# Kernel tuning notes

Measured on AMD Instinct MI355X. Metric: run time of the kernel, lower is better.

## Reference

```python
import jax, jax.numpy as jnp
import numpy as np

DIM = 256
WIN = 8          # window height == width
HEADS = 8
HEAD_DIM = DIM // HEADS
NW = 64          # number of windows per image
B_IMG = 16
N = WIN * WIN    # 64 tokens per window
B_ = B_IMG * NW  # 1024


def _relative_position_index():
    # matches torch.meshgrid default (ij) indexing
    coords = np.stack(np.meshgrid(np.arange(WIN), np.arange(WIN), indexing='ij'))  # [2,Wh,Ww]
    flat = coords.reshape(2, -1)                                # [2,N]
    rel = flat[:, :, None] - flat[:, None, :]                   # [2,N,N]
    rel = rel.transpose(1, 2, 0).copy()                         # [N,N,2]
    rel[:, :, 0] += WIN - 1
    rel[:, :, 1] += WIN - 1
    rel[:, :, 0] *= 2 * WIN - 1
    return rel.sum(-1).astype(np.int32)                         # [N,N]


def setup_inputs() -> dict:
    key = jax.random.key(0)
    ks = jax.random.split(key, 24)
    std = 0.02

    def lin(i):
        W = jax.random.normal(ks[i], (DIM, DIM), jnp.float32) * std
        b = jax.random.normal(ks[i + 1], (DIM,), jnp.float32) * std
        return W, b

    Wq, bq = lin(0)
    Wk, bk = lin(2)
    Wv, bv = lin(4)
    Wvs, bvs = lin(6)      # v_scale
    Wvh, bvh = lin(8)      # v_shift
    Wpx, bpx = lin(10)     # proj_x
    Wps, bps = lin(12)     # proj_scale
    Wph, bph = lin(14)     # proj_shift

    bias_table = jax.random.normal(ks[16], ((2 * WIN - 1) * (2 * WIN - 1), HEADS), jnp.float32) * std
    rel_idx = jnp.asarray(_relative_position_index())

    q_input = jax.random.normal(ks[17], (B_, N, DIM), jnp.float32)
    k_input = jax.random.normal(ks[18], (B_, N, DIM), jnp.float32)
    v_input = jax.random.normal(ks[19], (B_, N, DIM), jnp.float32)
    scale_in = jax.random.normal(ks[20], (B_, N, DIM), jnp.float32)
    shift_in = jax.random.normal(ks[21], (B_, N, DIM), jnp.float32)

    # shifted-window style mask: 0 where attendable, large negative otherwise
    u = jax.random.uniform(ks[22], (NW, N, N), jnp.float32)
    mask = jnp.where(u < 0.15, -100.0, 0.0).astype(jnp.float32)

    return {
        'q_input': q_input, 'k_input': k_input, 'v_input': v_input,
        'scale_in': scale_in, 'shift_in': shift_in, 'mask': mask,
        'Wq': Wq, 'bq': bq, 'Wk': Wk, 'bk': bk, 'Wv': Wv, 'bv': bv,
        'Wvs': Wvs, 'bvs': bvs, 'Wvh': Wvh, 'bvh': bvh,
        'Wpx': Wpx, 'bpx': bpx, 'Wps': Wps, 'bps': bps, 'Wph': Wph, 'bph': bph,
        'bias_table': bias_table, 'rel_idx': rel_idx,
    }


def reference(q_input, k_input, v_input, scale_in, shift_in, mask,
              Wq, bq, Wk, bk, Wv, bv, Wvs, bvs, Wvh, bvh,
              Wpx, bpx, Wps, bps, Wph, bph, bias_table, rel_idx):
    B, Ntok, C = q_input.shape
    scale = HEAD_DIM ** -0.5

    def to_heads(x, W, b):
        # nn.Linear: x @ W.T + b, then split heads -> [B, H, N, hd]
        return (x @ W.T + b).reshape(B, Ntok, HEADS, HEAD_DIM).transpose(0, 2, 1, 3)

    q = to_heads(q_input, Wq, bq) * scale
    k = to_heads(k_input, Wk, bk)
    v = to_heads(v_input, Wv, bv)
    v_scale = to_heads(scale_in, Wvs, bvs)
    v_shift = to_heads(shift_in, Wvh, bvh)

    attn = jnp.einsum('bhnd,bhmd->bhnm', q, k)                    # [B,H,N,N]
    rel_bias = bias_table[rel_idx]                                # [N,N,H] gather
    attn = attn + rel_bias.transpose(2, 0, 1)[None]               # add per-head bias

    nW = mask.shape[0]
    attn = attn.reshape(B // nW, nW, HEADS, Ntok, Ntok) + mask[None, :, None]
    attn = jax.nn.softmax(attn.reshape(B, HEADS, Ntok, Ntok), axis=-1)

    def out_proj(val, Wp, bp):
        o = jnp.einsum('bhnm,bhmd->bhnd', attn, val)
        o = o.transpose(0, 2, 1, 3).reshape(B, Ntok, C)
        return o @ Wp.T + bp

    x_out = out_proj(v, Wpx, bpx)
    scale_out = out_proj(v_scale, Wps, bps)
    shift_out = out_proj(v_shift, Wph, bph)
    return (x_out, scale_out, shift_out)
```

## Files before the change

### kernel.cpp

```cpp
#include <hip/hip_runtime.h>


typedef __attribute__((ext_vector_type(8))) __bf16 bf16x8;
typedef __attribute__((ext_vector_type(4))) float f32x4;
typedef __attribute__((ext_vector_type(4))) unsigned short u16x4;

__device__ __forceinline__ unsigned short f2bf(float f) {
  return __builtin_bit_cast(unsigned short, (__bf16)f);
}
__device__ __forceinline__ unsigned pk2(float lo, float hi) {
  return (unsigned)f2bf(lo) | ((unsigned)f2bf(hi) << 16);
}
__device__ __forceinline__ int swz256(int row, int col) {
  return row * 256 + (col ^ ((row & 31) << 3));
}
__device__ __forceinline__ f32x4 mfma16(bf16x8 a, bf16x8 b, f32x4 c) {
  return __builtin_amdgcn_mfma_f32_16x16x32_bf16(a, b, c, 0, 0, 0);
}

__global__ void pack_weights(const float* __restrict__ W0, const float* __restrict__ W1,
                             const float* __restrict__ W2, const float* __restrict__ W3,
                             const float* __restrict__ W4, const float* __restrict__ W5,
                             const float* __restrict__ W6, const float* __restrict__ W7,
                             unsigned short* __restrict__ pk) {
  int t = blockIdx.x * 256 + threadIdx.x;
  int mat = t >> 13;
  int w   = (t >> 11) & 3;
  int blk = (t >> 9) & 3;
  int kc  = (t >> 6) & 7;
  int l   = t & 63;
  const float* W = (mat == 0) ? W0 : (mat == 1) ? W1 : (mat == 2) ? W2 : (mat == 3) ? W3
                 : (mat == 4) ? W4 : (mat == 5) ? W5 : (mat == 6) ? W6 : W7;
  const float* src = W + (64 * w + 16 * blk + (l & 15)) * 256 + 32 * kc + 8 * (l >> 4);
  unsigned short* dst = pk + (size_t)t * 8;
#pragma unroll
  for (int i = 0; i < 8; ++i) dst[i] = f2bf(src[i]);
}

__global__ void make_bmt(const float* __restrict__ mask, const float* __restrict__ btab,
                         const int* __restrict__ ridx, float* __restrict__ bmt) {
  int t = blockIdx.x * 256 + threadIdx.x;
  int r  = t & 3;
  int l  = (t >> 2) & 63;
  int mf = (t >> 8) & 3;
  int nf = (t >> 10) & 3;
  int h  = (t >> 12) & 7;
  int wi = t >> 15;
  int q = 16 * nf + (l & 15);
  int k = 16 * mf + 4 * (l >> 4) + r;
  bmt[t] = mask[(wi * 64 + q) * 64 + k] + btab[ridx[q * 64 + k] * 8 + h];
}

__device__ __forceinline__ bf16x8 butterfly(f32x4 C0, f32x4 C1, int c4, int r16) {
  unsigned a0 = pk2(C0[0], C0[1]), a1 = pk2(C0[2], C0[3]);
  unsigned b0 = pk2(C1[0], C1[1]), b1 = pk2(C1[2], C1[3]);
  int src0 = (((2 * c4) & 3) << 4) + r16;
  int src1 = (((2 * c4 + 1) & 3) << 4) + r16;
  unsigned A0 = (unsigned)__shfl((int)a0, src0);
  unsigned A1 = (unsigned)__shfl((int)a1, src0);
  unsigned A2 = (unsigned)__shfl((int)a0, src1);
  unsigned A3 = (unsigned)__shfl((int)a1, src1);
  unsigned B0 = (unsigned)__shfl((int)b0, src0);
  unsigned B1 = (unsigned)__shfl((int)b1, src0);
  unsigned B2 = (unsigned)__shfl((int)b0, src1);
  unsigned B3 = (unsigned)__shfl((int)b1, src1);
  bool hi = c4 >= 2;
  union { unsigned u[4]; bf16x8 v; } r;
  r.u[0] = hi ? B0 : A0;
  r.u[1] = hi ? B1 : A1;
  r.u[2] = hi ? B2 : A2;
  r.u[3] = hi ? B3 : A3;
  return r.v;
}

__device__ __forceinline__ void load8(f32x4 r[8], const float* __restrict__ X,
                                      int b, int tid, int half) {
  const f32x4* src = reinterpret_cast<const f32x4*>(X + (size_t)b * 16384) + half * 2048;
#pragma unroll
  for (int it = 0; it < 8; ++it) r[it] = src[it * 256 + tid];
}
__device__ __forceinline__ void write8(unsigned short* T, const f32x4 r[8], int tid, int half) {
#pragma unroll
  for (int it = 0; it < 8; ++it) {
    int f = half * 2048 + it * 256 + tid;
    int row = f >> 6;
    int col = (f & 63) << 2;
    u16x4 p;
    p[0] = f2bf(r[it][0]); p[1] = f2bf(r[it][1]);
    p[2] = f2bf(r[it][2]); p[3] = f2bf(r[it][3]);
    *reinterpret_cast<u16x4*>(T + swz256(row, col)) = p;
  }
}
__device__ __forceinline__ void stage_tile(unsigned short* T, const float* __restrict__ X,
                                           int b, int tid) {
  f32x4 r[8];
  load8(r, X, b, tid, 0);
  write8(T, r, tid, 0);
  load8(r, X, b, tid, 1);
  write8(T, r, tid, 1);
}

__device__ __forceinline__ const unsigned short* pwBase(const unsigned short* pk,
                                                        int mat, int w2) {
  return pk + mat * 65536 + w2 * 16384;
}

__device__ __forceinline__ void projT2(const unsigned short* __restrict__ T,
                                       const unsigned short* __restrict__ pw,
                                       const float* __restrict__ bias, float scale,
                                       int lane, int w2, bf16x8 fA[4], bf16x8 fB[4]) {
  const int r16 = lane & 15, c4 = lane >> 4;
  f32x4 z = {0.f, 0.f, 0.f, 0.f};
  f32x4 acc[4][4];
#pragma unroll
  for (int j = 0; j < 4; ++j)
#pragma unroll
    for (int nf = 0; nf < 4; ++nf) acc[j][nf] = z;
#pragma unroll
  for (int kc = 0; kc < 8; ++kc) {
    bf16x8 aw[4], bx[4];
#pragma unroll
    for (int j = 0; j < 4; ++j)
      aw[j] = *reinterpret_cast<const bf16x8*>(pw + (j * 8 + kc) * 512 + lane * 8);
#pragma unroll
    for (int nf = 0; nf < 4; ++nf)
      bx[nf] = *reinterpret_cast<const bf16x8*>(T + swz256(16 * nf + r16, 32 * kc + 8 * c4));
#pragma unroll
    for (int j = 0; j < 4; ++j)
#pragma unroll
      for (int nf = 0; nf < 4; ++nf) acc[j][nf] = mfma16(aw[j], bx[nf], acc[j][nf]);
  }
#pragma unroll
  for (int j = 0; j < 4; ++j) {
    f32x4 b4 = *reinterpret_cast<const f32x4*>(bias + 64 * w2 + 16 * j + 4 * c4);
#pragma unroll
    for (int nf = 0; nf < 4; ++nf)
#pragma unroll
      for (int r = 0; r < 4; ++r) acc[j][nf][r] = (acc[j][nf][r] + b4[r]) * scale;
  }
#pragma unroll
  for (int nf = 0; nf < 4; ++nf) {
    fA[nf] = butterfly(acc[0][nf], acc[1][nf], c4, r16);
    fB[nf] = butterfly(acc[2][nf], acc[3][nf], c4, r16);
  }
}

__device__ __forceinline__ void attn_head(const bf16x8 Qf[4], const bf16x8 Kf[4],
                                          const float* __restrict__ bmb,
                                          int lane, bf16x8 Pf[4][2]) {
  const int r16 = lane & 15, c4 = lane >> 4;
  f32x4 z = {0.f, 0.f, 0.f, 0.f};
#pragma unroll
  for (int qb = 0; qb < 4; ++qb) {
    f32x4 s[4];
#pragma unroll
    for (int t = 0; t < 4; ++t) s[t] = mfma16(Kf[t], Qf[qb], z);
    float mx = -1e30f;
#pragma unroll
    for (int t = 0; t < 4; ++t) {
      f32x4 bm4 = *reinterpret_cast<const f32x4*>(bmb + (((qb * 4 + t) * 64 + lane) << 2));
#pragma unroll
      for (int r = 0; r < 4; ++r) {
        s[t][r] += bm4[r];
        mx = fmaxf(mx, s[t][r]);
      }
    }
    mx = fmaxf(mx, __shfl_xor(mx, 16));
    mx = fmaxf(mx, __shfl_xor(mx, 32));
    float sum = 0.f;
#pragma unroll
    for (int t = 0; t < 4; ++t)
#pragma unroll
      for (int r = 0; r < 4; ++r) {
        s[t][r] = __expf(s[t][r] - mx);
        sum += s[t][r];
      }
    sum += __shfl_xor(sum, 16);
    sum += __shfl_xor(sum, 32);
    float inv = 1.0f / sum;
#pragma unroll
    for (int kc = 0; kc < 2; ++kc) {
      f32x4 p0, p1;
#pragma unroll
      for (int r = 0; r < 4; ++r) {
        p0[r] = s[2 * kc][r] * inv;
        p1[r] = s[2 * kc + 1][r] * inv;
      }
      Pf[qb][kc] = butterfly(p0, p1, c4, r16);
    }
  }
}

__device__ __forceinline__ void projN64(const unsigned short* __restrict__ T,
                                        const unsigned short* __restrict__ pw,
                                        int lane, f32x4 acc[4][4]) {
  const int r16 = lane & 15, c4 = lane >> 4;
  f32x4 z = {0.f, 0.f, 0.f, 0.f};
#pragma unroll
  for (int mf = 0; mf < 4; ++mf)
#pragma unroll
    for (int nf = 0; nf < 4; ++nf) acc[mf][nf] = z;
#pragma unroll
  for (int kc = 0; kc < 8; ++kc) {
    bf16x8 a[4], bb[4];
#pragma unroll
    for (int mf = 0; mf < 4; ++mf)
      a[mf] = *reinterpret_cast<const bf16x8*>(T + swz256(16 * mf + r16, 32 * kc + 8 * c4));
#pragma unroll
    for (int nf = 0; nf < 4; ++nf)
      bb[nf] = *reinterpret_cast<const bf16x8*>(pw + (nf * 8 + kc) * 512 + lane * 8);
#pragma unroll
    for (int mf = 0; mf < 4; ++mf)
#pragma unroll
      for (int nf = 0; nf < 4; ++nf) acc[mf][nf] = mfma16(a[mf], bb[nf], acc[mf][nf]);
  }
}

__device__ __forceinline__ void vFrag2(f32x4 acc[4][4], const float* __restrict__ bias,
                                       int lane, int w2, bf16x8 VfA[2][2], bf16x8 VfB[2][2]) {
  const int r16 = lane & 15, c4 = lane >> 4;
#pragma unroll
  for (int nf = 0; nf < 4; ++nf) {
    float bb = bias[64 * w2 + 16 * nf + r16];
#pragma unroll
    for (int mf = 0; mf < 4; ++mf)
#pragma unroll
      for (int r = 0; r < 4; ++r) acc[mf][nf][r] += bb;
  }
#pragma unroll
  for (int nf = 0; nf < 2; ++nf) {
    VfA[0][nf] = butterfly(acc[0][nf], acc[1][nf], c4, r16);
    VfA[1][nf] = butterfly(acc[2][nf], acc[3][nf], c4, r16);
    VfB[0][nf] = butterfly(acc[0][nf + 2], acc[1][nf + 2], c4, r16);
    VfB[1][nf] = butterfly(acc[2][nf + 2], acc[3][nf + 2], c4, r16);
  }
}

__device__ __forceinline__ void pv_store(const bf16x8 Pf[4][2], const bf16x8 Vf[2][2],
                                         unsigned short* OS, int lane, int h) {
  const int r16 = lane & 15, c4 = lane >> 4;
  f32x4 z = {0.f, 0.f, 0.f, 0.f};
  f32x4 o[4][2];
#pragma unroll
  for (int qb = 0; qb < 4; ++qb)
#pragma unroll
    for (int nf = 0; nf < 2; ++nf) o[qb][nf] = z;
#pragma unroll
  for (int kc = 0; kc < 2; ++kc)
#pragma unroll
    for (int qb = 0; qb < 4; ++qb)
#pragma unroll
      for (int nf = 0; nf < 2; ++nf)
        o[qb][nf] = mfma16(Pf[qb][kc], Vf[kc][nf], o[qb][nf]);
#pragma unroll
  for (int qb = 0; qb < 4; ++qb)
#pragma unroll
    for (int nf = 0; nf < 2; ++nf)
#pragma unroll
      for (int r = 0; r < 4; ++r)
        OS[swz256(16 * qb + 4 * c4 + r, 32 * h + 16 * nf + r16)] = f2bf(o[qb][nf][r]);
}

__device__ __forceinline__ void outProj64(const unsigned short* __restrict__ OS,
                                          const unsigned short* __restrict__ pw,
                                          const float* __restrict__ bias,
                                          float* __restrict__ dst, int lane, int w2) {
  const int r16 = lane & 15, c4 = lane >> 4;
  f32x4 acc[4][4];
  projN64(OS, pw, lane, acc);
#pragma unroll
  for (int nf = 0; nf < 4; ++nf) {
    float bb = bias[64 * w2 + 16 * nf + r16];
#pragma unroll
    for (int mf = 0; mf < 4; ++mf)
#pragma unroll
      for (int r = 0; r < 4; ++r)
        dst[(16 * mf + 4 * c4 + r) * 256 + 64 * w2 + 16 * nf + r16] = acc[mf][nf][r] + bb;
  }
}

__global__ __launch_bounds__(256, 2) void win_attn(
    const float* __restrict__ gq, const float* __restrict__ gk, const float* __restrict__ gv,
    const float* __restrict__ gsc, const float* __restrict__ gsh,
    const unsigned short* __restrict__ pk,
    const float* __restrict__ b_q, const float* __restrict__ b_k, const float* __restrict__ b_v,
    const float* __restrict__ b_vs, const float* __restrict__ b_vh,
    const float* __restrict__ b_px, const float* __restrict__ b_ps, const float* __restrict__ b_ph,
    const float* __restrict__ bmt, float* __restrict__ out) {
  __shared__ __align__(16) unsigned short sm[32768];
  unsigned short* XS = sm;
  unsigned short* OS = sm + 16384;

  const int b    = blockIdx.x;
  const int tid  = threadIdx.x;
  const int lane = tid & 63;
  const int w2   = tid >> 6;
  const int wi   = b & 63;

  bf16x8 PfA[4][2], PfB[4][2];

  stage_tile(XS, gq, b, tid);
  stage_tile(OS, gk, b, tid);
  __syncthreads();

  {
    bf16x8 QfA[4], QfB[4], KfA[4], KfB[4];
    projT2(XS, pwBase(pk, 0, w2), b_q, 0.17677669529663687f, lane, w2, QfA, QfB);
    __syncthreads();

    projT2(OS, pwBase(pk, 1, w2), b_k, 1.0f, lane, w2, KfA, KfB);
    attn_head(QfA, KfA, bmt + ((size_t)(wi * 8 + 2 * w2) << 12), lane, PfA);
    attn_head(QfB, KfB, bmt + ((size_t)(wi * 8 + 2 * w2 + 1) << 12), lane, PfB);
    stage_tile(XS, gv, b, tid);
  }
  __syncthreads();

  {
    f32x4 acc[4][4];
    projN64(XS, pwBase(pk, 2, w2), lane, acc);
    bf16x8 VfA[2][2], VfB[2][2];
    vFrag2(acc, b_v, lane, w2, VfA, VfB);
    pv_store(PfA, VfA, OS, lane, 2 * w2);
    pv_store(PfB, VfB, OS, lane, 2 * w2 + 1);
  }
  __syncthreads();

  outProj64(OS, pwBase(pk, 5, w2), b_px, out + (size_t)b * 16384, lane, w2);
  stage_tile(XS, gsc, b, tid);
  __syncthreads();

  {
    f32x4 acc[4][4];
    projN64(XS, pwBase(pk, 3, w2), lane, acc);
    bf16x8 VfA[2][2], VfB[2][2];
    vFrag2(acc, b_vs, lane, w2, VfA, VfB);
    pv_store(PfA, VfA, OS, lane, 2 * w2);
    pv_store(PfB, VfB, OS, lane, 2 * w2 + 1);
  }
  __syncthreads();

  outProj64(OS, pwBase(pk, 6, w2), b_ps, out + 16777216 + (size_t)b * 16384, lane, w2);
  stage_tile(XS, gsh, b, tid);
  __syncthreads();

  {
    f32x4 acc[4][4];
    projN64(XS, pwBase(pk, 4, w2), lane, acc);
    bf16x8 VfA[2][2], VfB[2][2];
    vFrag2(acc, b_vh, lane, w2, VfA, VfB);
    pv_store(PfA, VfA, OS, lane, 2 * w2);
    pv_store(PfB, VfB, OS, lane, 2 * w2 + 1);
  }
  __syncthreads();

  outProj64(OS, pwBase(pk, 7, w2), b_ph, out + 33554432 + (size_t)b * 16384, lane, w2);
}

extern "C" void kernel_launch(void* const* d_in, const int* in_sizes, int n_in,
                              void* d_out, int out_size, void* d_ws, size_t ws_size,
                              hipStream_t stream) {
  const float* Xq   = (const float*)d_in[0];
  const float* Xk   = (const float*)d_in[1];
  const float* Xv   = (const float*)d_in[2];
  const float* Xsc  = (const float*)d_in[3];
  const float* Xsh  = (const float*)d_in[4];
  const float* mask = (const float*)d_in[5];
  const float* Wq   = (const float*)d_in[6];  const float* bq  = (const float*)d_in[7];
  const float* Wk   = (const float*)d_in[8];  const float* bk  = (const float*)d_in[9];
  const float* Wv   = (const float*)d_in[10]; const float* bv  = (const float*)d_in[11];
  const float* Wvs  = (const float*)d_in[12]; const float* bvs = (const float*)d_in[13];
  const float* Wvh  = (const float*)d_in[14]; const float* bvh = (const float*)d_in[15];
  const float* Wpx  = (const float*)d_in[16]; const float* bpx = (const float*)d_in[17];
  const float* Wps  = (const float*)d_in[18]; const float* bps = (const float*)d_in[19];
  const float* Wph  = (const float*)d_in[20]; const float* bph = (const float*)d_in[21];
  const float* btab = (const float*)d_in[22];
  const int*   ridx = (const int*)d_in[23];

  unsigned short* pk = (unsigned short*)d_ws;
  float* bmt = (float*)((char*)d_ws + (size_t)8 * 65536 * 2);

  pack_weights<<<256, 256, 0, stream>>>(Wq, Wk, Wv, Wvs, Wvh, Wpx, Wps, Wph, pk);
  make_bmt<<<8192, 256, 0, stream>>>(mask, btab, ridx, bmt);
  win_attn<<<1024, 256, 0, stream>>>(Xq, Xk, Xv, Xsc, Xsh, pk,
                                     bq, bk, bv, bvs, bvh, bpx, bps, bph,
                                     bmt, (float*)d_out);
}
```

Before: 261.0 us.

## Split fused window attention into projection and attention/output kernels

Replaces the single fused kernel with two kernels when the workspace is large enough. The first runs the five input projections as 5120 independent blocks and writes bf16 MFMA fragments to global memory. The second runs one wave per head with 512 threads to do attention and the three output projections. This buys more parallelism and lower per-block register pressure, at the cost of an extra round trip of about 170MB of bf16 intermediates through global memory. The original fused kernel remains as a fallback when the workspace is too small.

```diff
diff --git a/kernel.cpp b/kernel.cpp
--- a/kernel.cpp
+++ b/kernel.cpp
@@ -100,8 +100,8 @@
   write8(T, r, tid, 1);
 }
 
-__device__ __forceinline__ const unsigned short* pwBase(const unsigned short* pk,
-                                                        int mat, int w2) {
+__device__ __forceinline__ const unsigned short* pwBase7(const unsigned short* pk,
+                                                         int mat, int w2) {
   return pk + mat * 65536 + w2 * 16384;
 }
 
@@ -261,6 +261,48 @@
         OS[swz256(16 * qb + 4 * c4 + r, 32 * h + 16 * nf + r16)] = f2bf(o[qb][nf][r]);
 }
 
+__device__ __forceinline__ void projN32(const unsigned short* __restrict__ T,
+                                        const unsigned short* __restrict__ pw,
+                                        int lane, f32x4 acc[4][2]) {
+  const int r16 = lane & 15, c4 = lane >> 4;
+  f32x4 z = {0.f, 0.f, 0.f, 0.f};
+#pragma unroll
+  for (int mf = 0; mf < 4; ++mf)
+#pragma unroll
+    for (int nf = 0; nf < 2; ++nf) acc[mf][nf] = z;
+#pragma unroll
+  for (int kc = 0; kc < 8; ++kc) {
+    bf16x8 a[4], bb[2];
+#pragma unroll
+    for (int mf = 0; mf < 4; ++mf)
+      a[mf] = *reinterpret_cast<const bf16x8*>(T + swz256(16 * mf + r16, 32 * kc + 8 * c4));
+#pragma unroll
+    for (int nf = 0; nf < 2; ++nf)
+      bb[nf] = *reinterpret_cast<const bf16x8*>(pw + nf * 4096 + kc * 512 + lane * 8);
+#pragma unroll
+    for (int mf = 0; mf < 4; ++mf)
+#pragma unroll
+      for (int nf = 0; nf < 2; ++nf) acc[mf][nf] = mfma16(a[mf], bb[nf], acc[mf][nf]);
+  }
+}
+__device__ __forceinline__ void outProj(const unsigned short* __restrict__ OS,
+                                        const unsigned short* __restrict__ pw,
+                                        const float* __restrict__ bias,
+                                        float* __restrict__ dst, int lane, int w) {
+  const int r16 = lane & 15, c4 = lane >> 4;
+  f32x4 acc[4][2];
+  projN32(OS, pw, lane, acc);
+#pragma unroll
+  for (int nf = 0; nf < 2; ++nf) {
+    float bb = bias[32 * w + 16 * nf + r16];
+#pragma unroll
+    for (int mf = 0; mf < 4; ++mf)
+#pragma unroll
+      for (int r = 0; r < 4; ++r)
+        dst[(16 * mf + 4 * c4 + r) * 256 + 32 * w + 16 * nf + r16] = acc[mf][nf][r] + bb;
+  }
+}
+
 __device__ __forceinline__ void outProj64(const unsigned short* __restrict__ OS,
                                           const unsigned short* __restrict__ pw,
                                           const float* __restrict__ bias,
@@ -279,7 +321,106 @@
   }
 }
 
-__global__ __launch_bounds__(256, 2) void win_attn(
+__global__ __launch_bounds__(256, 4) void proj5(
+    const float* __restrict__ gq, const float* __restrict__ gk,
+    const float* __restrict__ gv, const float* __restrict__ gsc,
+    const float* __restrict__ gsh, const unsigned short* __restrict__ pk,
+    const float* __restrict__ b_q, const float* __restrict__ b_k,
+    const float* __restrict__ b_v, const float* __restrict__ b_vs,
+    const float* __restrict__ b_vh,
+    unsigned short* __restrict__ qf, unsigned short* __restrict__ kf,
+    unsigned short* __restrict__ vf) {
+  __shared__ __align__(16) unsigned short XS[16384];
+  const int bid = blockIdx.x;
+  const int mat = bid >> 10;
+  const int win = bid & 1023;
+  const int tid = threadIdx.x;
+  const int lane = tid & 63;
+  const int w2 = tid >> 6;
+  const float* X = (mat == 0) ? gq : (mat == 1) ? gk : (mat == 2) ? gv
+                 : (mat == 3) ? gsc : gsh;
+  stage_tile(XS, X, win, tid);
+  __syncthreads();
+  if (mat < 2) {
+    bf16x8 fA[4], fB[4];
+    projT2(XS, pwBase7(pk, mat, w2), mat == 0 ? b_q : b_k,
+           mat == 0 ? 0.17677669529663687f : 1.0f, lane, w2, fA, fB);
+    unsigned short* dst = (mat == 0 ? qf : kf) + (size_t)win * 16384 + lane * 8;
+#pragma unroll
+    for (int nf = 0; nf < 4; ++nf) {
+      *reinterpret_cast<bf16x8*>(dst + (2 * w2) * 2048 + nf * 512) = fA[nf];
+      *reinterpret_cast<bf16x8*>(dst + (2 * w2 + 1) * 2048 + nf * 512) = fB[nf];
+    }
+  } else {
+    f32x4 acc[4][4];
+    projN64(XS, pwBase7(pk, mat, w2), lane, acc);
+    bf16x8 VfA[2][2], VfB[2][2];
+    vFrag2(acc, mat == 2 ? b_v : (mat == 3 ? b_vs : b_vh), lane, w2, VfA, VfB);
+    unsigned short* dst = vf + (size_t)(mat - 2) * 16777216 + (size_t)win * 16384 + lane * 8;
+#pragma unroll
+    for (int kc = 0; kc < 2; ++kc)
+#pragma unroll
+      for (int nf = 0; nf < 2; ++nf) {
+        *reinterpret_cast<bf16x8*>(dst + (2 * w2) * 2048 + (kc * 2 + nf) * 512) = VfA[kc][nf];
+        *reinterpret_cast<bf16x8*>(dst + (2 * w2 + 1) * 2048 + (kc * 2 + nf) * 512) = VfB[kc][nf];
+      }
+  }
+}
+
+__global__ __launch_bounds__(512, 4) void attn_out(
+    const unsigned short* __restrict__ qf, const unsigned short* __restrict__ kf,
+    const unsigned short* __restrict__ vf, const unsigned short* __restrict__ pk,
+    const float* __restrict__ b_px, const float* __restrict__ b_ps,
+    const float* __restrict__ b_ph, const float* __restrict__ bmt,
+    float* __restrict__ out) {
+  __shared__ __align__(16) unsigned short OS[16384];
+  const int b = blockIdx.x;
+  const int tid = threadIdx.x;
+  const int lane = tid & 63;
+  const int w = tid >> 6;
+  const int wi = b & 63;
+  const size_t fb = (size_t)b * 16384 + w * 2048 + lane * 8;
+
+  bf16x8 Qf[4], Kf[4], Pf[4][2], VfA[2][2], VfB[2][2];
+#pragma unroll
+  for (int nf = 0; nf < 4; ++nf) {
+    Qf[nf] = *reinterpret_cast<const bf16x8*>(qf + fb + nf * 512);
+    Kf[nf] = *reinterpret_cast<const bf16x8*>(kf + fb + nf * 512);
+  }
+#pragma unroll
+  for (int kc = 0; kc < 2; ++kc)
+#pragma unroll
+    for (int nf = 0; nf < 2; ++nf)
+      VfA[kc][nf] = *reinterpret_cast<const bf16x8*>(vf + fb + (kc * 2 + nf) * 512);
+
+  attn_head(Qf, Kf, bmt + ((size_t)(wi * 8 + w) << 12), lane, Pf);
+
+  pv_store(Pf, VfA, OS, lane, w);
+  __syncthreads();
+#pragma unroll
+  for (int kc = 0; kc < 2; ++kc)
+#pragma unroll
+    for (int nf = 0; nf < 2; ++nf)
+      VfB[kc][nf] = *reinterpret_cast<const bf16x8*>(vf + 16777216 + fb + (kc * 2 + nf) * 512);
+  outProj(OS, pk + 5 * 65536 + w * 8192, b_px, out + (size_t)b * 16384, lane, w);
+  __syncthreads();
+
+  pv_store(Pf, VfB, OS, lane, w);
+  __syncthreads();
+#pragma unroll
+  for (int kc = 0; kc < 2; ++kc)
+#pragma unroll
+    for (int nf = 0; nf < 2; ++nf)
+      VfA[kc][nf] = *reinterpret_cast<const bf16x8*>(vf + 2 * 16777216 + fb + (kc * 2 + nf) * 512);
+  outProj(OS, pk + 6 * 65536 + w * 8192, b_ps, out + 16777216 + (size_t)b * 16384, lane, w);
+  __syncthreads();
+
+  pv_store(Pf, VfA, OS, lane, w);
+  __syncthreads();
+  outProj(OS, pk + 7 * 65536 + w * 8192, b_ph, out + 33554432 + (size_t)b * 16384, lane, w);
+}
+
+__global__ __launch_bounds__(256, 2) void win_attn_fused(
     const float* __restrict__ gq, const float* __restrict__ gk, const float* __restrict__ gv,
     const float* __restrict__ gsc, const float* __restrict__ gsh,
     const unsigned short* __restrict__ pk,
@@ -290,70 +431,59 @@
   __shared__ __align__(16) unsigned short sm[32768];
   unsigned short* XS = sm;
   unsigned short* OS = sm + 16384;
-
-  const int b    = blockIdx.x;
-  const int tid  = threadIdx.x;
+  const int b = blockIdx.x;
+  const int tid = threadIdx.x;
   const int lane = tid & 63;
-  const int w2   = tid >> 6;
-  const int wi   = b & 63;
-
+  const int w2 = tid >> 6;
+  const int wi = b & 63;
   bf16x8 PfA[4][2], PfB[4][2];
-
   stage_tile(XS, gq, b, tid);
   stage_tile(OS, gk, b, tid);
   __syncthreads();
-
   {
     bf16x8 QfA[4], QfB[4], KfA[4], KfB[4];
-    projT2(XS, pwBase(pk, 0, w2), b_q, 0.17677669529663687f, lane, w2, QfA, QfB);
+    projT2(XS, pwBase7(pk, 0, w2), b_q, 0.17677669529663687f, lane, w2, QfA, QfB);
     __syncthreads();
-
-    projT2(OS, pwBase(pk, 1, w2), b_k, 1.0f, lane, w2, KfA, KfB);
+    projT2(OS, pwBase7(pk, 1, w2), b_k, 1.0f, lane, w2, KfA, KfB);
     attn_head(QfA, KfA, bmt + ((size_t)(wi * 8 + 2 * w2) << 12), lane, PfA);
     attn_head(QfB, KfB, bmt + ((size_t)(wi * 8 + 2 * w2 + 1) << 12), lane, PfB);
     stage_tile(XS, gv, b, tid);
   }
   __syncthreads();
-
   {
     f32x4 acc[4][4];
-    projN64(XS, pwBase(pk, 2, w2), lane, acc);
+    projN64(XS, pwBase7(pk, 2, w2), lane, acc);
     bf16x8 VfA[2][2], VfB[2][2];
     vFrag2(acc, b_v, lane, w2, VfA, VfB);
     pv_store(PfA, VfA, OS, lane, 2 * w2);
     pv_store(PfB, VfB, OS, lane, 2 * w2 + 1);
   }
   __syncthreads();
-
-  outProj64(OS, pwBase(pk, 5, w2), b_px, out + (size_t)b * 16384, lane, w2);
+  outProj64(OS, pwBase7(pk, 5, w2), b_px, out + (size_t)b * 16384, lane, w2);
   stage_tile(XS, gsc, b, tid);
   __syncthreads();
-
   {
     f32x4 acc[4][4];
-    projN64(XS, pwBase(pk, 3, w2), lane, acc);
+    projN64(XS, pwBase7(pk, 3, w2), lane, acc);
     bf16x8 VfA[2][2], VfB[2][2];
     vFrag2(acc, b_vs, lane, w2, VfA, VfB);
     pv_store(PfA, VfA, OS, lane, 2 * w2);
     pv_store(PfB, VfB, OS, lane, 2 * w2 + 1);
   }
   __syncthreads();
-
-  outProj64(OS, pwBase(pk, 6, w2), b_ps, out + 16777216 + (size_t)b * 16384, lane, w2);
+  outProj64(OS, pwBase7(pk, 6, w2), b_ps, out + 16777216 + (size_t)b * 16384, lane, w2);
   stage_tile(XS, gsh, b, tid);
   __syncthreads();
-
   {
     f32x4 acc[4][4];
-    projN64(XS, pwBase(pk, 4, w2), lane, acc);
+    projN64(XS, pwBase7(pk, 4, w2), lane, acc);
     bf16x8 VfA[2][2], VfB[2][2];
     vFrag2(acc, b_vh, lane, w2, VfA, VfB);
     pv_store(PfA, VfA, OS, lane, 2 * w2);
     pv_store(PfB, VfB, OS, lane, 2 * w2 + 1);
   }
   __syncthreads();
-
-  outProj64(OS, pwBase(pk, 7, w2), b_ph, out + 33554432 + (size_t)b * 16384, lane, w2);
+  outProj64(OS, pwBase7(pk, 7, w2), b_ph, out + 33554432 + (size_t)b * 16384, lane, w2);
 }
 
 extern "C" void kernel_launch(void* const* d_in, const int* in_sizes, int n_in,
@@ -376,12 +506,25 @@
   const float* btab = (const float*)d_in[22];
   const int*   ridx = (const int*)d_in[23];
 
-  unsigned short* pk = (unsigned short*)d_ws;
-  float* bmt = (float*)((char*)d_ws + (size_t)8 * 65536 * 2);
+  char* ws = (char*)d_ws;
+  unsigned short* pk = (unsigned short*)ws;
+  float* bmt = (float*)(ws + (size_t)1048576);
+  unsigned short* qf = (unsigned short*)(ws + (size_t)9437184);
+  unsigned short* kf = (unsigned short*)(ws + (size_t)9437184 + 33554432);
+  unsigned short* vf = (unsigned short*)(ws + (size_t)9437184 + 67108864);
+  const size_t need = (size_t)9437184 + 67108864 + 100663296;
 
   pack_weights<<<256, 256, 0, stream>>>(Wq, Wk, Wv, Wvs, Wvh, Wpx, Wps, Wph, pk);
   make_bmt<<<8192, 256, 0, stream>>>(mask, btab, ridx, bmt);
-  win_attn<<<1024, 256, 0, stream>>>(Xq, Xk, Xv, Xsc, Xsh, pk,
-                                     bq, bk, bv, bvs, bvh, bpx, bps, bph,
-                                     bmt, (float*)d_out);
-}
+
+  if (ws_size >= need) {
+    proj5<<<5120, 256, 0, stream>>>(Xq, Xk, Xv, Xsc, Xsh, pk,
+                                    bq, bk, bv, bvs, bvh, qf, kf, vf);
+    attn_out<<<1024, 512, 0, stream>>>(qf, kf, vf, pk, bpx, bps, bph,
+                                       bmt, (float*)d_out);
+  } else {
+    win_attn_fused<<<1024, 256, 0, stream>>>(Xq, Xk, Xv, Xsc, Xsh, pk,
+                                             bq, bk, bv, bvs, bvh, bpx, bps, bph,
+                                             bmt, (float*)d_out);
+  }
+}
```

Result: slower. 318.7 us (+22.1%).

## Split each window across two blocks by query half, prefetch inputs, raise MFMA priority

Applied to the files above, without the earlier changes.

Each block now handles half of the query rows of one window, so the grid doubles to 2048 blocks. Each block projects only its half of Q and half of the outputs, but still computes full K and all three V projections. Global loads of the next input tile are issued into registers ahead of the matrix work, using a larger triple-buffered shared memory layout, and s_setprio is raised around MFMA loops. The aim is more parallelism and better overlap of loads with compute. The cost is redundant K/V projection work in both halves, more shared memory per block, and more registers held by the prefetch.

```diff
diff --git a/kernel.cpp b/kernel.cpp
--- a/kernel.cpp
+++ b/kernel.cpp
@@ -74,8 +74,8 @@
 }
 
 __device__ __forceinline__ void load8(f32x4 r[8], const float* __restrict__ X,
-                                      int b, int tid, int half) {
-  const f32x4* src = reinterpret_cast<const f32x4*>(X + (size_t)b * 16384) + half * 2048;
+                                      int win, int tid, int half) {
+  const f32x4* src = reinterpret_cast<const f32x4*>(X + (size_t)win * 16384) + half * 2048;
 #pragma unroll
   for (int it = 0; it < 8; ++it) r[it] = src[it * 256 + tid];
 }
@@ -92,16 +92,33 @@
   }
 }
 __device__ __forceinline__ void stage_tile(unsigned short* T, const float* __restrict__ X,
-                                           int b, int tid) {
+                                           int win, int tid) {
+  f32x4 r0[8], r1[8];
+  load8(r0, X, win, tid, 0);
+  load8(r1, X, win, tid, 1);
+  write8(T, r0, tid, 0);
+  write8(T, r1, tid, 1);
+}
+__device__ __forceinline__ void stage_half(unsigned short* BO, const float* __restrict__ X,
+                                           int win, int hf, int tid) {
   f32x4 r[8];
-  load8(r, X, b, tid, 0);
-  write8(T, r, tid, 0);
-  load8(r, X, b, tid, 1);
-  write8(T, r, tid, 1);
-}
-
-__device__ __forceinline__ const unsigned short* pwBase(const unsigned short* pk,
-                                                        int mat, int w2) {
+  const f32x4* src = reinterpret_cast<const f32x4*>(X + (size_t)win * 16384 + hf * 8192);
+#pragma unroll
+  for (int it = 0; it < 8; ++it) r[it] = src[it * 256 + tid];
+#pragma unroll
+  for (int it = 0; it < 8; ++it) {
+    int f = it * 256 + tid;
+    int row = f >> 6;
+    int col = (f & 63) << 2;
+    u16x4 p;
+    p[0] = f2bf(r[it][0]); p[1] = f2bf(r[it][1]);
+    p[2] = f2bf(r[it][2]); p[3] = f2bf(r[it][3]);
+    *reinterpret_cast<u16x4*>(BO + swz256(row, col)) = p;
+  }
+}
+
+__device__ __forceinline__ const unsigned short* pwBase7(const unsigned short* pk,
+                                                         int mat, int w2) {
   return pk + mat * 65536 + w2 * 16384;
 }
 
@@ -116,6 +133,7 @@
   for (int j = 0; j < 4; ++j)
 #pragma unroll
     for (int nf = 0; nf < 4; ++nf) acc[j][nf] = z;
+  __builtin_amdgcn_s_setprio(1);
 #pragma unroll
   for (int kc = 0; kc < 8; ++kc) {
     bf16x8 aw[4], bx[4];
@@ -130,6 +148,7 @@
 #pragma unroll
       for (int nf = 0; nf < 4; ++nf) acc[j][nf] = mfma16(aw[j], bx[nf], acc[j][nf]);
   }
+  __builtin_amdgcn_s_setprio(0);
 #pragma unroll
   for (int j = 0; j < 4; ++j) {
     f32x4 b4 = *reinterpret_cast<const f32x4*>(bias + 64 * w2 + 16 * j + 4 * c4);
@@ -145,20 +164,65 @@
   }
 }
 
-__device__ __forceinline__ void attn_head(const bf16x8 Qf[4], const bf16x8 Kf[4],
-                                          const float* __restrict__ bmb,
-                                          int lane, bf16x8 Pf[4][2]) {
-  const int r16 = lane & 15, c4 = lane >> 4;
-  f32x4 z = {0.f, 0.f, 0.f, 0.f};
-#pragma unroll
-  for (int qb = 0; qb < 4; ++qb) {
+__device__ __forceinline__ void projT2q(const unsigned short* __restrict__ BO,
+                                        const unsigned short* __restrict__ pw,
+                                        const float* __restrict__ bias, float scale,
+                                        int lane, int w2, bf16x8 fA[2], bf16x8 fB[2]) {
+  const int r16 = lane & 15, c4 = lane >> 4;
+  f32x4 z = {0.f, 0.f, 0.f, 0.f};
+  f32x4 acc[4][2];
+#pragma unroll
+  for (int j = 0; j < 4; ++j)
+#pragma unroll
+    for (int nf = 0; nf < 2; ++nf) acc[j][nf] = z;
+  __builtin_amdgcn_s_setprio(1);
+#pragma unroll
+  for (int kc = 0; kc < 8; ++kc) {
+    bf16x8 aw[4], bx[2];
+#pragma unroll
+    for (int j = 0; j < 4; ++j)
+      aw[j] = *reinterpret_cast<const bf16x8*>(pw + (j * 8 + kc) * 512 + lane * 8);
+#pragma unroll
+    for (int nf = 0; nf < 2; ++nf)
+      bx[nf] = *reinterpret_cast<const bf16x8*>(BO + swz256(16 * nf + r16, 32 * kc + 8 * c4));
+#pragma unroll
+    for (int j = 0; j < 4; ++j)
+#pragma unroll
+      for (int nf = 0; nf < 2; ++nf) acc[j][nf] = mfma16(aw[j], bx[nf], acc[j][nf]);
+  }
+  __builtin_amdgcn_s_setprio(0);
+#pragma unroll
+  for (int j = 0; j < 4; ++j) {
+    f32x4 b4 = *reinterpret_cast<const f32x4*>(bias + 64 * w2 + 16 * j + 4 * c4);
+#pragma unroll
+    for (int nf = 0; nf < 2; ++nf)
+#pragma unroll
+      for (int r = 0; r < 4; ++r) acc[j][nf][r] = (acc[j][nf][r] + b4[r]) * scale;
+  }
+#pragma unroll
+  for (int nf = 0; nf < 2; ++nf) {
+    fA[nf] = butterfly(acc[0][nf], acc[1][nf], c4, r16);
+    fB[nf] = butterfly(acc[2][nf], acc[3][nf], c4, r16);
+  }
+}
+
+__device__ __forceinline__ void attn_half(const bf16x8 Qf2[2], const bf16x8 Kf[4],
+                                          const float* __restrict__ bmb, int hf,
+                                          int lane, bf16x8 Pf[2][2]) {
+  const int r16 = lane & 15, c4 = lane >> 4;
+  f32x4 z = {0.f, 0.f, 0.f, 0.f};
+#pragma unroll
+  for (int qb2 = 0; qb2 < 2; ++qb2) {
     f32x4 s[4];
-#pragma unroll
-    for (int t = 0; t < 4; ++t) s[t] = mfma16(Kf[t], Qf[qb], z);
+    __builtin_amdgcn_s_setprio(1);
+#pragma unroll
+    for (int t = 0; t < 4; ++t) s[t] = mfma16(Kf[t], Qf2[qb2], z);
+    __builtin_amdgcn_s_setprio(0);
+    const int nfq = 2 * hf + qb2;
     float mx = -1e30f;
 #pragma unroll
     for (int t = 0; t < 4; ++t) {
-      f32x4 bm4 = *reinterpret_cast<const f32x4*>(bmb + (((qb * 4 + t) * 64 + lane) << 2));
+      f32x4 bm4 = *reinterpret_cast<const f32x4*>(bmb + (((nfq * 4 + t) * 64 + lane) << 2));
 #pragma unroll
       for (int r = 0; r < 4; ++r) {
         s[t][r] += bm4[r];
@@ -186,7 +250,7 @@
         p0[r] = s[2 * kc][r] * inv;
         p1[r] = s[2 * kc + 1][r] * inv;
       }
-      Pf[qb][kc] = butterfly(p0, p1, c4, r16);
+      Pf[qb2][kc] = butterfly(p0, p1, c4, r16);
     }
   }
 }
@@ -200,6 +264,7 @@
   for (int mf = 0; mf < 4; ++mf)
 #pragma unroll
     for (int nf = 0; nf < 4; ++nf) acc[mf][nf] = z;
+  __builtin_amdgcn_s_setprio(1);
 #pragma unroll
   for (int kc = 0; kc < 8; ++kc) {
     bf16x8 a[4], bb[4];
@@ -214,6 +279,7 @@
 #pragma unroll
       for (int nf = 0; nf < 4; ++nf) acc[mf][nf] = mfma16(a[mf], bb[nf], acc[mf][nf]);
   }
+  __builtin_amdgcn_s_setprio(0);
 }
 
 __device__ __forceinline__ void vFrag2(f32x4 acc[4][4], const float* __restrict__ bias,
@@ -236,43 +302,63 @@
   }
 }
 
-__device__ __forceinline__ void pv_store(const bf16x8 Pf[4][2], const bf16x8 Vf[2][2],
-                                         unsigned short* OS, int lane, int h) {
-  const int r16 = lane & 15, c4 = lane >> 4;
-  f32x4 z = {0.f, 0.f, 0.f, 0.f};
-  f32x4 o[4][2];
-#pragma unroll
-  for (int qb = 0; qb < 4; ++qb)
-#pragma unroll
-    for (int nf = 0; nf < 2; ++nf) o[qb][nf] = z;
+__device__ __forceinline__ void pv_half(const bf16x8 Pf[2][2], const bf16x8 Vf[2][2],
+                                        unsigned short* BO, int lane, int h) {
+  const int r16 = lane & 15, c4 = lane >> 4;
+  f32x4 z = {0.f, 0.f, 0.f, 0.f};
+  f32x4 o[2][2];
+#pragma unroll
+  for (int qb2 = 0; qb2 < 2; ++qb2)
+#pragma unroll
+    for (int nf = 0; nf < 2; ++nf) o[qb2][nf] = z;
 #pragma unroll
   for (int kc = 0; kc < 2; ++kc)
 #pragma unroll
-    for (int qb = 0; qb < 4; ++qb)
+    for (int qb2 = 0; qb2 < 2; ++qb2)
 #pragma unroll
       for (int nf = 0; nf < 2; ++nf)
-        o[qb][nf] = mfma16(Pf[qb][kc], Vf[kc][nf], o[qb][nf]);
-#pragma unroll
-  for (int qb = 0; qb < 4; ++qb)
+        o[qb2][nf] = mfma16(Pf[qb2][kc], Vf[kc][nf], o[qb2][nf]);
+#pragma unroll
+  for (int qb2 = 0; qb2 < 2; ++qb2)
 #pragma unroll
     for (int nf = 0; nf < 2; ++nf)
 #pragma unroll
       for (int r = 0; r < 4; ++r)
-        OS[swz256(16 * qb + 4 * c4 + r, 32 * h + 16 * nf + r16)] = f2bf(o[qb][nf][r]);
-}
-
-__device__ __forceinline__ void outProj64(const unsigned short* __restrict__ OS,
-                                          const unsigned short* __restrict__ pw,
-                                          const float* __restrict__ bias,
-                                          float* __restrict__ dst, int lane, int w2) {
-  const int r16 = lane & 15, c4 = lane >> 4;
-  f32x4 acc[4][4];
-  projN64(OS, pw, lane, acc);
+        BO[swz256(16 * qb2 + 4 * c4 + r, 32 * h + 16 * nf + r16)] = f2bf(o[qb2][nf][r]);
+}
+
+__device__ __forceinline__ void outProj_half(const unsigned short* __restrict__ BO,
+                                             const unsigned short* __restrict__ pw,
+                                             const float* __restrict__ bias,
+                                             float* __restrict__ dst, int lane, int w2) {
+  const int r16 = lane & 15, c4 = lane >> 4;
+  f32x4 z = {0.f, 0.f, 0.f, 0.f};
+  f32x4 acc[2][4];
+#pragma unroll
+  for (int mf = 0; mf < 2; ++mf)
+#pragma unroll
+    for (int nf = 0; nf < 4; ++nf) acc[mf][nf] = z;
+  __builtin_amdgcn_s_setprio(1);
+#pragma unroll
+  for (int kc = 0; kc < 8; ++kc) {
+    bf16x8 a[2], bb[4];
+#pragma unroll
+    for (int mf = 0; mf < 2; ++mf)
+      a[mf] = *reinterpret_cast<const bf16x8*>(BO + swz256(16 * mf + r16, 32 * kc + 8 * c4));
+#pragma unroll
+    for (int nf = 0; nf < 4; ++nf)
+      bb[nf] = *reinterpret_cast<const bf16x8*>(pw + (nf * 8 + kc) * 512 + lane * 8);
+#pragma unroll
+    for (int mf = 0; mf < 2; ++mf)
+#pragma unroll
+      for (int nf = 0; nf < 4; ++nf) acc[mf][nf] = mfma16(a[mf], bb[nf], acc[mf][nf]);
+  }
+  __builtin_amdgcn_s_setprio(0);
 #pragma unroll
   for (int nf = 0; nf < 4; ++nf) {
     float bb = bias[64 * w2 + 16 * nf + r16];
 #pragma unroll
-    for (int mf = 0; mf < 4; ++mf)
+    for (int mf = 0; mf < 2; ++mf)
 #pragma unroll
       for (int r = 0; r < 4; ++r)
         dst[(16 * mf + 4 * c4 + r) * 256 + 64 * w2 + 16 * nf + r16] = acc[mf][nf][r] + bb;
@@ -287,73 +373,90 @@
     const float* __restrict__ b_vs, const float* __restrict__ b_vh,
     const float* __restrict__ b_px, const float* __restrict__ b_ps, const float* __restrict__ b_ph,
     const float* __restrict__ bmt, float* __restrict__ out) {
-  __shared__ __align__(16) unsigned short sm[32768];
-  unsigned short* XS = sm;
-  unsigned short* OS = sm + 16384;
-
-  const int b    = blockIdx.x;
+  __shared__ __align__(16) unsigned short sm[40960];
+  unsigned short* BO = sm;
+  unsigned short* A  = sm + 8192;
+  unsigned short* B  = sm + 24576;
+
+  const int bid  = blockIdx.x;
+  const int win  = (bid & 7) | ((bid >> 4) << 3);
+  const int hf   = (bid >> 3) & 1;
   const int tid  = threadIdx.x;
   const int lane = tid & 63;
   const int w2   = tid >> 6;
-  const int wi   = b & 63;
-
-  bf16x8 PfA[4][2], PfB[4][2];
-
-  stage_tile(XS, gq, b, tid);
-  stage_tile(OS, gk, b, tid);
+  const int wi   = win & 63;
+
+  bf16x8 PfA[2][2], PfB[2][2];
+  bf16x8 VfA[2][2], VfB[2][2];
+
+  const size_t outBase = (size_t)win * 16384 + (size_t)hf * 8192;
+
+  stage_half(BO, gq, win, hf, tid);
+  stage_tile(A, gk, win, tid);
   __syncthreads();
 
   {
-    bf16x8 QfA[4], QfB[4], KfA[4], KfB[4];
-    projT2(XS, pwBase(pk, 0, w2), b_q, 0.17677669529663687f, lane, w2, QfA, QfB);
-    __syncthreads();
-
-    projT2(OS, pwBase(pk, 1, w2), b_k, 1.0f, lane, w2, KfA, KfB);
-    attn_head(QfA, KfA, bmt + ((size_t)(wi * 8 + 2 * w2) << 12), lane, PfA);
-    attn_head(QfB, KfB, bmt + ((size_t)(wi * 8 + 2 * w2 + 1) << 12), lane, PfB);
-    stage_tile(XS, gv, b, tid);
-  }
-  __syncthreads();
-
+    f32x4 r0[8], r1[8];
+    load8(r0, gv, win, tid, 0);
+    load8(r1, gv, win, tid, 1);
+    bf16x8 KfA[4], KfB[4], QfA[2], QfB[2];
+    projT2(A, pwBase7(pk, 1, w2), b_k, 1.0f, lane, w2, KfA, KfB);
+    projT2q(BO, pwBase7(pk, 0, w2), b_q, 0.17677669529663687f, lane, w2, QfA, QfB);
+    attn_half(QfA, KfA, bmt + ((size_t)(wi * 8 + 2 * w2) << 12), hf, lane, PfA);
+    attn_half(QfB, KfB, bmt + ((size_t)(wi * 8 + 2 * w2 + 1) << 12), hf, lane, PfB);
+    write8(B, r0, tid, 0);
+    write8(B, r1, tid, 1);
+  }
+  __syncthreads();
+
+  {
+    f32x4 r0[8], r1[8];
+    load8(r0, gsc, win, tid, 0);
+    load8(r1, gsc, win, tid, 1);
+    {
+      f32x4 acc[4][4];
+      projN64(B, pwBase7(pk, 2, w2), lane, acc);
+      vFrag2(acc, b_v, lane, w2, VfA, VfB);
+    }
+    pv_half(PfA, VfA, BO, lane, 2 * w2);
+    pv_half(PfB, VfB, BO, lane, 2 * w2 + 1);
+    write8(A, r0, tid, 0);
+    write8(A, r1, tid, 1);
+  }
+  __syncthreads();
+
+  outProj_half(BO, pwBase7(pk, 5, w2), b_px, out + outBase, lane, w2);
   {
     f32x4 acc[4][4];
-    projN64(XS, pwBase(pk, 2, w2), lane, acc);
-    bf16x8 VfA[2][2], VfB[2][2];
-    vFrag2(acc, b_v, lane, w2, VfA, VfB);
-    pv_store(PfA, VfA, OS, lane, 2 * w2);
-    pv_store(PfB, VfB, OS, lane, 2 * w2 + 1);
-  }
-  __syncthreads();
-
-  outProj64(OS, pwBase(pk, 5, w2), b_px, out + (size_t)b * 16384, lane, w2);
-  stage_tile(XS, gsc, b, tid);
-  __syncthreads();
-
+    projN64(A, pwBase7(pk, 3, w2), lane, acc);
+    vFrag2(acc, b_vs, lane, w2, VfA, VfB);
+  }
+  __syncthreads();
+
+  pv_half(PfA, VfA, BO, lane, 2 * w2);
+  pv_half(PfB, VfB, BO, lane, 2 * w2 + 1);
+  {
+    f32x4 r0[8], r1[8];
+    load8(r0, gsh, win, tid, 0);
+    load8(r1, gsh, win, tid, 1);
+    write8(B, r0, tid, 0);
+    write8(B, r1, tid, 1);
+  }
+  __syncthreads();
+
+  outProj_half(BO, pwBase7(pk, 6, w2), b_ps, out + 16777216 + outBase, lane, w2);
   {
     f32x4 acc[4][4];
-    projN64(XS, pwBase(pk, 3, w2), lane, acc);
-    bf16x8 VfA[2][2], VfB[2][2];
-    vFrag2(acc, b_vs, lane, w2, VfA, VfB);
-    pv_store(PfA, VfA, OS, lane, 2 * w2);
-    pv_store(PfB, VfB, OS, lane, 2 * w2 + 1);
-  }
-  __syncthreads();
-
-  outProj64(OS, pwBase(pk, 6, w2), b_ps, out + 16777216 + (size_t)b * 16384, lane, w2);
-  stage_tile(XS, gsh, b, tid);
-  __syncthreads();
-
-  {
-    f32x4 acc[4][4];
-    projN64(XS, pwBase(pk, 4, w2), lane, acc);
-    bf16x8 VfA[2][2], VfB[2][2];
+    projN64(B, pwBase7(pk, 4, w2), lane, acc);
     vFrag2(acc, b_vh, lane, w2, VfA, VfB);
-    pv_store(PfA, VfA, OS, lane, 2 * w2);
-    pv_store(PfB, VfB, OS, lane, 2 * w2 + 1);
-  }
-  __syncthreads();
-
-  outProj64(OS, pwBase(pk, 7, w2), b_ph, out + 33554432 + (size_t)b * 16384, lane, w2);
+  }
+  __syncthreads();
+
+  pv_half(PfA, VfA, BO, lane, 2 * w2);
+  pv_half(PfB, VfB, BO, lane, 2 * w2 + 1);
+  __syncthreads();
+
+  outProj_half(BO, pwBase7(pk, 7, w2), b_ph, out + 33554432 + outBase, lane, w2);
 }
 
 extern "C" void kernel_launch(void* const* d_in, const int* in_sizes, int n_in,
@@ -381,7 +484,7 @@
 
   pack_weights<<<256, 256, 0, stream>>>(Wq, Wk, Wv, Wvs, Wvh, Wpx, Wps, Wph, pk);
   make_bmt<<<8192, 256, 0, stream>>>(mask, btab, ridx, bmt);
-  win_attn<<<1024, 256, 0, stream>>>(Xq, Xk, Xv, Xsc, Xsh, pk,
+  win_attn<<<2048, 256, 0, stream>>>(Xq, Xk, Xv, Xsc, Xsh, pk,
                                      bq, bk, bv, bvs, bvh, bpx, bps, bph,
                                      bmt, (float*)d_out);
 }
```

Measured after the change: 257.2 us. No clear change (-1.4%).
